# Performance work log

Hardware: AMD Instinct MI355X
Metric: run time of the kernel (lower is better)

Reference implementation:

```python
import jax, jax.numpy as jnp
import numpy as np

N, T, GX, GY, GQ = 16, 64, 256, 256, 256   # solutions, timesteps, source grid, query grid
H, D = 4, 8                                 # attention heads / head dim
SIGMA = 0.2
LY_MIN, LY_MAX = 30.0, 120.0
CU_REF, NI_REF = 0.0029, 0.0018
LX = 100.0


def setup_inputs() -> dict:
    key = jax.random.key(0)
    ks = jax.random.split(key, 7)
    lys = jax.random.uniform(ks[0], (N,), minval=40.0, maxval=110.0)
    ccu = jax.random.uniform(ks[1], (N,), minval=0.001, maxval=CU_REF)
    cni = jax.random.uniform(ks[2], (N,), minval=0.0005, maxval=NI_REF)
    params = jnp.stack([lys, ccu, cni], axis=1).astype(jnp.float32)  # [N,3] raw (Ly, C_Cu, C_Ni)
    x_grids = jnp.tile(jnp.linspace(0.0, LX, GX, dtype=jnp.float32)[None], (N, 1))      # [N,GX]
    y_grids = lys[:, None] * jnp.linspace(0.0, 1.0, GY, dtype=jnp.float32)[None]        # [N,GY]
    c1_src = jax.random.normal(ks[3], (N, T, GX, GY), dtype=jnp.float32)
    c2_src = jax.random.normal(ks[4], (N, T, GX, GY), dtype=jnp.float32)
    Wq_w = 0.1 * jax.random.normal(ks[5], (H * D, 3), dtype=jnp.float32)
    Wk_w = 0.1 * jax.random.normal(ks[6], (H * D, 3), dtype=jnp.float32)
    Wq_b = jnp.zeros((H * D,), jnp.float32)
    Wk_b = jnp.zeros((H * D,), jnp.float32)
    return dict(c1_src=c1_src, c2_src=c2_src, x_grids=x_grids, y_grids=y_grids,
                params=params, Wq_w=Wq_w, Wq_b=Wq_b, Wk_w=Wk_w, Wk_b=Wk_b,
                ly_target=jnp.float32(75.0), c_cu_target=jnp.float32(0.0029),
                c_ni_target=jnp.float32(0.0018))


def _bilinear(c, xg, yg, qx, qy):
    """Linear interp on rectilinear grid, fill_value=0 out of bounds.
    c: [T,Gx,Gy], xg: [Gx], yg: [Gy], qx/qy: [P] -> [T,P]."""
    ix = jnp.clip(jnp.searchsorted(xg, qx, side='right') - 1, 0, xg.shape[0] - 2)
    iy = jnp.clip(jnp.searchsorted(yg, qy, side='right') - 1, 0, yg.shape[0] - 2)
    x0, x1 = xg[ix], xg[ix + 1]
    y0, y1 = yg[iy], yg[iy + 1]
    fx = (qx - x0) / (x1 - x0)
    fy = (qy - y0) / (y1 - y0)
    c00 = c[:, ix, iy]
    c10 = c[:, ix + 1, iy]
    c01 = c[:, ix, iy + 1]
    c11 = c[:, ix + 1, iy + 1]
    v = ((1 - fx) * (1 - fy)) * c00 + (fx * (1 - fy)) * c10 \
        + ((1 - fx) * fy) * c01 + (fx * fy) * c11
    inb = (qx >= xg[0]) & (qx <= xg[-1]) & (qy >= yg[0]) & (qy <= yg[-1])
    return jnp.where(inb[None, :], v, 0.0)


def _forward(c1_src, c2_src, x_grids, y_grids, params, Wq_w, Wq_b, Wk_w, Wk_b,
             ly_target, c_cu_target, c_ni_target):
    # --- parameter normalization (same constants as original) ---
    p = jnp.stack([(params[:, 0] - LY_MIN) / (LY_MAX - LY_MIN),
                   params[:, 1] / CU_REF,
                   params[:, 2] / NI_REF], axis=1)                     # [N,3]
    tgt = jnp.stack([(ly_target - LY_MIN) / (LY_MAX - LY_MIN),
                     c_cu_target / CU_REF,
                     c_ni_target / NI_REF])[None, :]                   # [1,3]
    # --- tiny multi-head attention weights ---
    q = (tgt @ Wq_w.T + Wq_b).reshape(1, H, D)
    k = (p @ Wk_w.T + Wk_b).reshape(p.shape[0], H, D)
    attn = jnp.einsum('nhd,mhd->nmh', k, q) / np.sqrt(D).astype(np.float32)  # [N,1,H]
    attn_w = jax.nn.softmax(attn, axis=0).mean(axis=2).squeeze(1)            # [N]
    # --- gaussian spatial weights ---
    sw = jnp.exp(-0.5 * jnp.sum(((p - tgt) / SIGMA) ** 2, axis=1))
    sw = sw / sw.sum()
    w = attn_w * sw
    w = w / w.sum()
    w = jax.lax.stop_gradient(w)  # original detaches weights before interpolation
    # --- batched bilinear interpolation onto target grid ---
    Lx = x_grids[0, -1]
    unit = jnp.linspace(0.0, 1.0, GQ, dtype=jnp.float32)
    X, Y = jnp.meshgrid(unit * Lx, unit * ly_target, indexing='ij')    # [GQ,GQ]
    qx, qy = X.ravel(), Y.ravel()                                      # [P]
    ys = y_grids * (ly_target / params[:, 0])[:, None]                 # per-solution rescaled Y grids
    interp = jax.vmap(_bilinear, in_axes=(0, 0, 0, None, None))        # -> [N,T,P]
    c1 = jnp.einsum('n,ntp->tp', w, interp(c1_src, x_grids, ys, qx, qy)).reshape(T, GQ, GQ)
    c2 = jnp.einsum('n,ntp->tp', w, interp(c2_src, x_grids, ys, qx, qy)).reshape(T, GQ, GQ)
    # --- boundary conditions ---
    c1 = c1.at[:, :, 0].set(c_cu_target)
    c2 = c2.at[:, :, -1].set(c_ni_target)
    return jnp.stack([c1, c2]), w


def reference(c1_src, c2_src, x_grids, y_grids, params, Wq_w, Wq_b, Wk_w, Wk_b,
              ly_target, c_cu_target, c_ni_target):
    return _forward(c1_src, c2_src, x_grids, y_grids, params, Wq_w, Wq_b, Wk_w, Wk_b,
                    ly_target, c_cu_target, c_ni_target)
```

## Files before the change

### kernel.cpp

```cpp
#include <hip/hip_runtime.h>

#define N_SRC 16
#define T_DIM 64
#define GXD 256
#define GYD 256
#define GQD 256
#define HN 4
#define DN 8
#define TI 8
#define ROWS 12
#define ROWSV 10
#define NB 4
#define NPLANES (2 * N_SRC)
#define CHPP 3
#define USED_CHUNKS (ROWSV * 64)
#define PLANE_STRIDE ((size_t)T_DIM * GXD * GYD)
#define OUT_C_ELEMS (2 * T_DIM * GQD * GQD)

#define WS_IY   0
#define WS_WY0  16384
#define WS_WY1  32768
#define WS_IX   49152
#define WS_WX0  50176
#define WS_WX1  51200

__device__ __forceinline__ float unitv(int i) {
    return (i == GQD - 1) ? 1.0f : (float)i * (1.0f / 255.0f);
}

__global__ __launch_bounds__(256) void table_kernel(
    const float* __restrict__ xg, const float* __restrict__ yg,
    const float* __restrict__ params,
    const float* __restrict__ Wq_w, const float* __restrict__ Wq_b,
    const float* __restrict__ Wk_w, const float* __restrict__ Wk_b,
    const float* __restrict__ lyt_p, const float* __restrict__ ccut_p,
    const float* __restrict__ cnit_p,
    float* __restrict__ out_w, char* __restrict__ ws)
{
    __shared__ float xg_sm[GXD];
    __shared__ float ys_sm[N_SRC][GYD];
    __shared__ float w_sm[N_SRC];

    const int tid = threadIdx.x;
    const float lyt = *lyt_p;

    xg_sm[tid] = xg[tid];
    #pragma unroll
    for (int n = 0; n < N_SRC; ++n) {
        float s = lyt / params[n * 3 + 0];
        ys_sm[n][tid] = yg[n * GYD + tid] * s;
    }

    if (tid == 0) {
        const float ccut = *ccut_p, cnit = *cnit_p;
        float tgt[3];
        tgt[0] = (lyt - 30.0f) / 90.0f;
        tgt[1] = ccut / 0.0029f;
        tgt[2] = cnit / 0.0018f;
        float q[HN * DN];
        for (int hd = 0; hd < HN * DN; ++hd)
            q[hd] = tgt[0] * Wq_w[hd * 3 + 0] + tgt[1] * Wq_w[hd * 3 + 1] + tgt[2] * Wq_w[hd * 3 + 2] + Wq_b[hd];
        float p[N_SRC][3];
        float attn[N_SRC][HN];
        for (int n = 0; n < N_SRC; ++n) {
            p[n][0] = (params[n * 3 + 0] - 30.0f) / 90.0f;
            p[n][1] = params[n * 3 + 1] / 0.0029f;
            p[n][2] = params[n * 3 + 2] / 0.0018f;
            for (int h = 0; h < HN; ++h) {
                float acc = 0.0f;
                for (int d = 0; d < DN; ++d) {
                    int hd = h * DN + d;
                    float kv = p[n][0] * Wk_w[hd * 3 + 0] + p[n][1] * Wk_w[hd * 3 + 1] + p[n][2] * Wk_w[hd * 3 + 2] + Wk_b[hd];
                    acc += kv * q[hd];
                }
                attn[n][h] = acc / sqrtf(8.0f);
            }
        }
        float aw[N_SRC];
        for (int n = 0; n < N_SRC; ++n) aw[n] = 0.0f;
        for (int h = 0; h < HN; ++h) {
            float m = attn[0][h];
            for (int n = 1; n < N_SRC; ++n) m = fmaxf(m, attn[n][h]);
            float e[N_SRC], s = 0.0f;
            for (int n = 0; n < N_SRC; ++n) { e[n] = expf(attn[n][h] - m); s += e[n]; }
            for (int n = 0; n < N_SRC; ++n) aw[n] += e[n] / s;
        }
        for (int n = 0; n < N_SRC; ++n) aw[n] *= (1.0f / (float)HN);
        float sw[N_SRC], ss = 0.0f;
        for (int n = 0; n < N_SRC; ++n) {
            float d0 = (p[n][0] - tgt[0]) / 0.2f;
            float d1 = (p[n][1] - tgt[1]) / 0.2f;
            float d2 = (p[n][2] - tgt[2]) / 0.2f;
            sw[n] = expf(-0.5f * (d0 * d0 + d1 * d1 + d2 * d2));
            ss += sw[n];
        }
        float w[N_SRC], wsum = 0.0f;
        for (int n = 0; n < N_SRC; ++n) { w[n] = aw[n] * (sw[n] / ss); wsum += w[n]; }
        for (int n = 0; n < N_SRC; ++n) {
            float wf = w[n] / wsum;
            w_sm[n] = wf;
            out_w[n] = wf;
        }
    }
    __syncthreads();

    int*   iy_tab  = (int*)  (ws + WS_IY);
    float* wy0_tab = (float*)(ws + WS_WY0);
    float* wy1_tab = (float*)(ws + WS_WY1);
    int*   ix_tab  = (int*)  (ws + WS_IX);
    float* wx0_tab = (float*)(ws + WS_WX0);
    float* wx1_tab = (float*)(ws + WS_WX1);

    const int j = tid;
    const float qy = unitv(j) * lyt;
    #pragma unroll
    for (int n = 0; n < N_SRC; ++n) {
        int lo = 0, hi = GYD;
        while (lo < hi) { int mid = (lo + hi) >> 1; if (ys_sm[n][mid] <= qy) lo = mid + 1; else hi = mid; }
        int idx = lo - 1;
        idx = idx < 0 ? 0 : (idx > GYD - 2 ? GYD - 2 : idx);
        float y0 = ys_sm[n][idx], y1 = ys_sm[n][idx + 1];
        float fy = (qy - y0) / (y1 - y0);
        float vy = (qy >= ys_sm[n][0] && qy <= ys_sm[n][GYD - 1]) ? 1.0f : 0.0f;
        float wn = w_sm[n] * vy;
        iy_tab [n * GQD + j] = idx;
        wy0_tab[n * GQD + j] = wn * (1.0f - fy);
        wy1_tab[n * GQD + j] = wn * fy;
    }

    const float Lx = xg_sm[GXD - 1];
    const float qx = unitv(tid) * Lx;
    int lo = 0, hi = GXD;
    while (lo < hi) { int mid = (lo + hi) >> 1; if (xg_sm[mid] <= qx) lo = mid + 1; else hi = mid; }
    int ixi = lo - 1;
    ixi = ixi < 0 ? 0 : (ixi > GXD - 2 ? GXD - 2 : ixi);
    const float x0 = xg_sm[ixi], x1 = xg_sm[ixi + 1];
    const float fx = (qx - x0) / (x1 - x0);
    const float vx = (qx >= xg_sm[0] && qx <= xg_sm[GXD - 1]) ? 1.0f : 0.0f;
    ix_tab [tid] = ixi;
    wx0_tab[tid] = vx * (1.0f - fx);
    wx1_tab[tid] = vx * fx;
}

__device__ __forceinline__ void gl_lds16(const float* g, float* l) {
    __builtin_amdgcn_global_load_lds(
        (const __attribute__((address_space(1))) void*)g,
        (__attribute__((address_space(3))) void*)l, 16, 0, 0);
}

__global__ __launch_bounds__(256, 4) void fused_kernel(
    const float* __restrict__ c1, const float* __restrict__ c2,
    const float* __restrict__ ccut_p, const float* __restrict__ cnit_p,
    const char* __restrict__ ws, float* __restrict__ out)
{
    __shared__ float buf[NB][ROWS * GYD];

    const int tid = threadIdx.x;
    const int j = tid;
    const int i0 = blockIdx.x * TI;
    const int t = blockIdx.y;

    const int*   iy_tab  = (const int*)  (ws + WS_IY);
    const float* wy0_tab = (const float*)(ws + WS_WY0);
    const float* wy1_tab = (const float*)(ws + WS_WY1);
    const int*   ix_tab  = (const int*)  (ws + WS_IX);
    const float* wx0_tab = (const float*)(ws + WS_WX0);
    const float* wx1_tab = (const float*)(ws + WS_WX1);

    const int x0r = ix_tab[i0];
    int   dsel[TI];
    float wx0r[TI], wx1r[TI];
    #pragma unroll
    for (int ii = 0; ii < TI; ++ii) {
        int d = ix_tab[i0 + ii] - x0r - ii;
        dsel[ii] = d < -1 ? -1 : (d > 1 ? 1 : d);
        wx0r[ii] = wx0_tab[i0 + ii];
        wx1r[ii] = wx1_tab[i0 + ii];
    }

    int   iyr [N_SRC];
    float wy0r[N_SRC], wy1r[N_SRC];
    #pragma unroll
    for (int n = 0; n < N_SRC; ++n) {
        iyr [n] = iy_tab [n * GQD + j];
        wy0r[n] = wy0_tab[n * GQD + j];
        wy1r[n] = wy1_tab[n * GQD + j];
    }

    size_t soff[CHPP];
    int    ldst[CHPP];
    #pragma unroll
    for (int k = 0; k < CHPP; ++k) {
        int c  = tid + k * 256;
        int cc = c < USED_CHUNKS ? c : USED_CHUNKS - 1;
        int grow = x0r + (cc >> 6);
        grow = grow > GXD - 1 ? GXD - 1 : grow;
        soff[k] = (size_t)grow * GYD + ((cc & 63) << 2);
        ldst[k] = c << 2;
    }

    const size_t pbase = (size_t)t * (GXD * GYD);

    float acc1[TI], acc2[TI];
    #pragma unroll
    for (int ii = 0; ii < TI; ++ii) { acc1[ii] = 0.0f; acc2[ii] = 0.0f; }

#define STAGE(q) do {                                                          \
    const float* _s = (((q) & 1) ? c2 : c1) + pbase                            \
                      + (size_t)((q) >> 1) * PLANE_STRIDE;                     \
    float* _l = &buf[(q) & (NB - 1)][0];                                       \
    gl_lds16(_s + soff[0], _l + ldst[0]);                                      \
    gl_lds16(_s + soff[1], _l + ldst[1]);                                      \
    gl_lds16(_s + soff[2], _l + ldst[2]);                                      \
} while (0)

#define CONSUME(q, ACC) do {                                                   \
    const float* _B = &buf[(q) & (NB - 1)][0];                                 \
    const int _iy = iyr[(q) >> 1];                                             \
    const float _w0 = wy0r[(q) >> 1], _w1 = wy1r[(q) >> 1];                    \
    float _rv[ROWSV];                                                          \
    _Pragma("unroll")                                                          \
    for (int _r = 0; _r < ROWSV; ++_r)                                         \
        _rv[_r] = _w0 * _B[_r * GYD + _iy] + _w1 * _B[_r * GYD + _iy + 1];     \
    _Pragma("unroll")                                                          \
    for (int _ii = 0; _ii < TI; ++_ii) {                                       \
        const int _im1 = _ii > 0 ? _ii - 1 : 0;                                \
        const int _ip2 = _ii + 2 < ROWSV ? _ii + 2 : ROWSV - 1;                \
        const int _d = dsel[_ii];                                              \
        float _lo = _d == 0 ? _rv[_ii]     : (_d < 0 ? _rv[_im1] : _rv[_ii+1]);\
        float _hi = _d == 0 ? _rv[_ii + 1] : (_d < 0 ? _rv[_ii]  : _rv[_ip2]); \
        ACC[_ii] += wx0r[_ii] * _lo + wx1r[_ii] * _hi;                         \
    }                                                                          \
} while (0)

#define WAITQ(q) do {                                                          \
    if ((q) < NPLANES - 2)       asm volatile("s_waitcnt vmcnt(6)" ::: "memory"); \
    else if ((q) == NPLANES - 2) asm volatile("s_waitcnt vmcnt(3)" ::: "memory"); \
    else                         asm volatile("s_waitcnt vmcnt(0)" ::: "memory"); \
} while (0)

#define PLANE(q) do {                                                          \
    WAITQ(q);                                                                  \
    __builtin_amdgcn_s_barrier();                                              \
    __builtin_amdgcn_sched_barrier(0);                                         \
    if ((q) + 3 < NPLANES) STAGE((q) + 3);                                     \
    if (((q) & 1) == 0) CONSUME((q), acc1); else CONSUME((q), acc2);           \
} while (0)

    STAGE(0); STAGE(1); STAGE(2);

    PLANE(0);  PLANE(1);  PLANE(2);  PLANE(3);
    PLANE(4);  PLANE(5);  PLANE(6);  PLANE(7);
    PLANE(8);  PLANE(9);  PLANE(10); PLANE(11);
    PLANE(12); PLANE(13); PLANE(14); PLANE(15);
    PLANE(16); PLANE(17); PLANE(18); PLANE(19);
    PLANE(20); PLANE(21); PLANE(22); PLANE(23);
    PLANE(24); PLANE(25); PLANE(26); PLANE(27);
    PLANE(28); PLANE(29); PLANE(30); PLANE(31);

#undef PLANE
#undef WAITQ
#undef CONSUME
#undef STAGE

    const float ccut = *ccut_p, cnit = *cnit_p;
    #pragma unroll
    for (int ii = 0; ii < TI; ++ii) {
        const int i = i0 + ii;
        float o1 = acc1[ii];
        float o2 = acc2[ii];
        if (j == 0)       o1 = ccut;
        if (j == GQD - 1) o2 = cnit;
        __builtin_nontemporal_store(o1, &out[((size_t)t * GQD + i) * GQD + j]);
        __builtin_nontemporal_store(o2, &out[(((size_t)T_DIM + t) * GQD + i) * GQD + j]);
    }
}

extern "C" void kernel_launch(void* const* d_in, const int* in_sizes, int n_in,
                              void* d_out, int out_size, void* d_ws, size_t ws_size,
                              hipStream_t stream) {
    const float* c1     = (const float*)d_in[0];
    const float* c2     = (const float*)d_in[1];
    const float* xg     = (const float*)d_in[2];
    const float* yg     = (const float*)d_in[3];
    const float* params = (const float*)d_in[4];
    const float* Wq_w   = (const float*)d_in[5];
    const float* Wq_b   = (const float*)d_in[6];
    const float* Wk_w   = (const float*)d_in[7];
    const float* Wk_b   = (const float*)d_in[8];
    const float* lyt    = (const float*)d_in[9];
    const float* ccut   = (const float*)d_in[10];
    const float* cnit   = (const float*)d_in[11];
    float* out = (float*)d_out;
    float* out_w = out + OUT_C_ELEMS;
    char* ws = (char*)d_ws;

    table_kernel<<<1, 256, 0, stream>>>(xg, yg, params, Wq_w, Wq_b, Wk_w, Wk_b,
                                        lyt, ccut, cnit, out_w, ws);
    dim3 grid(GQD / TI, T_DIM);
    fused_kernel<<<grid, 256, 0, stream>>>(c1, c2, ccut, cnit, ws, out);
}
```

Measured before the change: 595.7 us.

## Shrink LDS ring to three buffers and stream per-source y-tables just in time

Reduces the LDS ring from four to three plane buffers, with prefetch distance two instead of three. The per-source y-interpolation tables are no longer preloaded into registers. They are loaded one source ahead into a small double-buffered register pair, and the two y weights are packed as float2. The aim is to cut LDS use and VGPR pressure so more blocks fit per CU. The cost is a shorter prefetch lead, table loads inside the main loop, and vmcnt waits that must be accounted carefully since table loads share the counter.

Result: slower. 778.7 us (+30.7%).

```diff
diff --git a/kernel.cpp b/kernel.cpp
--- a/kernel.cpp
+++ b/kernel.cpp
@@ -10,7 +10,7 @@
 #define TI 8
 #define ROWS 12
 #define ROWSV 10
-#define NB 4
+#define NB 3
 #define NPLANES (2 * N_SRC)
 #define CHPP 3
 #define USED_CHUNKS (ROWSV * 64)
@@ -18,8 +18,7 @@
 #define OUT_C_ELEMS (2 * T_DIM * GQD * GQD)
 
 #define WS_IY   0
-#define WS_WY0  16384
-#define WS_WY1  32768
+#define WS_WY01 16384
 #define WS_IX   49152
 #define WS_WX0  50176
 #define WS_WX1  51200
@@ -104,12 +103,11 @@
     }
     __syncthreads();
 
-    int*   iy_tab  = (int*)  (ws + WS_IY);
-    float* wy0_tab = (float*)(ws + WS_WY0);
-    float* wy1_tab = (float*)(ws + WS_WY1);
-    int*   ix_tab  = (int*)  (ws + WS_IX);
-    float* wx0_tab = (float*)(ws + WS_WX0);
-    float* wx1_tab = (float*)(ws + WS_WX1);
+    int*    iy_tab = (int*)   (ws + WS_IY);
+    float2* wy_tab = (float2*)(ws + WS_WY01);
+    int*    ix_tab = (int*)   (ws + WS_IX);
+    float*  wx0_tab = (float*)(ws + WS_WX0);
+    float*  wx1_tab = (float*)(ws + WS_WX1);
 
     const int j = tid;
     const float qy = unitv(j) * lyt;
@@ -123,9 +121,8 @@
         float fy = (qy - y0) / (y1 - y0);
         float vy = (qy >= ys_sm[n][0] && qy <= ys_sm[n][GYD - 1]) ? 1.0f : 0.0f;
         float wn = w_sm[n] * vy;
-        iy_tab [n * GQD + j] = idx;
-        wy0_tab[n * GQD + j] = wn * (1.0f - fy);
-        wy1_tab[n * GQD + j] = wn * fy;
+        iy_tab[n * GQD + j] = idx;
+        wy_tab[n * GQD + j] = make_float2(wn * (1.0f - fy), wn * fy);
     }
 
     const float Lx = xg_sm[GXD - 1];
@@ -160,12 +157,11 @@
     const int i0 = blockIdx.x * TI;
     const int t = blockIdx.y;
 
-    const int*   iy_tab  = (const int*)  (ws + WS_IY);
-    const float* wy0_tab = (const float*)(ws + WS_WY0);
-    const float* wy1_tab = (const float*)(ws + WS_WY1);
-    const int*   ix_tab  = (const int*)  (ws + WS_IX);
-    const float* wx0_tab = (const float*)(ws + WS_WX0);
-    const float* wx1_tab = (const float*)(ws + WS_WX1);
+    const int*    iy_tab = (const int*)   (ws + WS_IY);
+    const float2* wy_tab = (const float2*)(ws + WS_WY01);
+    const int*    ix_tab = (const int*)   (ws + WS_IX);
+    const float*  wx0_tab = (const float*)(ws + WS_WX0);
+    const float*  wx1_tab = (const float*)(ws + WS_WX1);
 
     const int x0r = ix_tab[i0];
     int   dsel[TI];
@@ -176,15 +172,6 @@
         dsel[ii] = d < -1 ? -1 : (d > 1 ? 1 : d);
         wx0r[ii] = wx0_tab[i0 + ii];
         wx1r[ii] = wx1_tab[i0 + ii];
-    }
-
-    int   iyr [N_SRC];
-    float wy0r[N_SRC], wy1r[N_SRC];
-    #pragma unroll
-    for (int n = 0; n < N_SRC; ++n) {
-        iyr [n] = iy_tab [n * GQD + j];
-        wy0r[n] = wy0_tab[n * GQD + j];
-        wy1r[n] = wy1_tab[n * GQD + j];
     }
 
     size_t soff[CHPP];
@@ -205,19 +192,29 @@
     #pragma unroll
     for (int ii = 0; ii < TI; ++ii) { acc1[ii] = 0.0f; acc2[ii] = 0.0f; }
 
+    int    tc_iy, tn_iy;
+    float2 tc_wy, tn_wy;
+
+#define FENCE asm volatile("" ::: "memory")
+
+#define TLOAD(n) do {                                                          \
+    tn_iy = iy_tab[(n) * GQD + j];                 \
+    tn_wy = wy_tab[(n) * GQD + j];                 \
+} while (0)
+
 #define STAGE(q) do {                                                          \
     const float* _s = (((q) & 1) ? c2 : c1) + pbase                            \
                       + (size_t)((q) >> 1) * PLANE_STRIDE;                     \
-    float* _l = &buf[(q) & (NB - 1)][0];                                       \
+    float* _l = &buf[(q) % NB][0];                                             \
     gl_lds16(_s + soff[0], _l + ldst[0]);                                      \
     gl_lds16(_s + soff[1], _l + ldst[1]);                                      \
     gl_lds16(_s + soff[2], _l + ldst[2]);                                      \
 } while (0)
 
 #define CONSUME(q, ACC) do {                                                   \
-    const float* _B = &buf[(q) & (NB - 1)][0];                                 \
-    const int _iy = iyr[(q) >> 1];                                             \
-    const float _w0 = wy0r[(q) >> 1], _w1 = wy1r[(q) >> 1];                    \
+    const float* _B = &buf[(q) % NB][0];                                       \
+    const int _iy = tc_iy;                                                     \
+    const float _w0 = tc_wy.x, _w1 = tc_wy.y;                                  \
     float _rv[ROWSV];                                                          \
     _Pragma("unroll")                                                          \
     for (int _r = 0; _r < ROWSV; ++_r)                                         \
@@ -234,20 +231,26 @@
 } while (0)
 
 #define WAITQ(q) do {                                                          \
-    if ((q) < NPLANES - 2)       asm volatile("s_waitcnt vmcnt(6)" ::: "memory"); \
-    else if ((q) == NPLANES - 2) asm volatile("s_waitcnt vmcnt(3)" ::: "memory"); \
-    else                         asm volatile("s_waitcnt vmcnt(0)" ::: "memory"); \
+    if ((q) == NPLANES - 1)  asm volatile("s_waitcnt vmcnt(0)" ::: "memory");  \
+    else if ((q) & 1)        asm volatile("s_waitcnt vmcnt(5)" ::: "memory");  \
+    else                     asm volatile("s_waitcnt vmcnt(3)" ::: "memory");  \
 } while (0)
 
 #define PLANE(q) do {                                                          \
     WAITQ(q);                                                                  \
     __builtin_amdgcn_s_barrier();                                              \
-    __builtin_amdgcn_sched_barrier(0);                                         \
-    if ((q) + 3 < NPLANES) STAGE((q) + 3);                                     \
+    FENCE;        \
+    if (((q) & 1) == 0) {                                                      \
+        tc_iy = tn_iy; tc_wy = tn_wy;                                          \
+        if ((((q) >> 1) + 1) < N_SRC) TLOAD(((q) >> 1) + 1);                   \
+    }                                                                          \
+    if ((q) + 2 < NPLANES) STAGE((q) + 2);                                     \
     if (((q) & 1) == 0) CONSUME((q), acc1); else CONSUME((q), acc2);           \
 } while (0)
 
-    STAGE(0); STAGE(1); STAGE(2);
+    TLOAD(0); FENCE;
+    STAGE(0); FENCE;
+    STAGE(1); FENCE;
 
     PLANE(0);  PLANE(1);  PLANE(2);  PLANE(3);
     PLANE(4);  PLANE(5);  PLANE(6);  PLANE(7);
@@ -262,6 +265,8 @@
 #undef WAITQ
 #undef CONSUME
 #undef STAGE
+#undef TLOAD
+#undef FENCE
 
     const float ccut = *ccut_p, cnit = *cnit_p;
     #pragma unroll
```
